# Kernel tuning notes

Hardware: AMD Instinct MI355X
Metric: run time of the kernel (lower is better)

The kernel has to match this reference:

```python
import jax, jax.numpy as jnp
import numpy as np


def _h(s):
    # Step function: 0 where s > 0, else 1 (zero gradient everywhere).
    return jnp.where(s > 0, 0.0, 1.0).astype(s.dtype)


def setup_inputs() -> dict:
    key = jax.random.key(0)
    k1, k2, k3 = jax.random.split(key, 3)
    B, T = 4096, 2048
    x = jax.random.normal(k1, (B, T, 1), dtype=jnp.float32)
    out_prev = jax.random.normal(k2, (B, 1, 1), dtype=jnp.float32)
    lstm_outs = jax.random.normal(k3, (B, T, 4), dtype=jnp.float32)
    return {"x": x, "out_prev": out_prev, "lstm_outs": lstm_outs}


def reference(x, out_prev, lstm_outs):
    # x: [B, T, 1], out_prev: [B, 1, 1] (only first step used), lstm_outs: [B, T, 4]
    xT = jnp.swapaxes(x, 0, 1)          # [T, B, 1]
    wT = jnp.swapaxes(lstm_outs, 0, 1)  # [T, B, 4]

    def step(prev, inputs):
        # prev: [B, 1]
        xt, wt = inputs                  # [B, 1], [B, 4]
        m_lo = wt[:, 0:1]
        m_up = wt[:, 1:2]
        c_lo = wt[:, 2:3]
        c_up = wt[:, 3:4]
        # h() arguments use detached weights in the original (grad is zero through
        # the step function anyway); stop_gradient kept for faithfulness.
        m_lo_d = jax.lax.stop_gradient(m_lo)
        m_up_d = jax.lax.stop_gradient(m_up)
        c_lo_d = jax.lax.stop_gradient(c_lo)
        c_up_d = jax.lax.stop_gradient(c_up)
        f1 = _h((m_lo_d * xt + m_lo_d * c_lo_d - prev) / m_lo_d)
        f2 = _h((prev - m_up_d * xt - m_up_d * c_up_d) / m_up_d)
        out = (m_lo * xt * f1 + m_lo * c_lo * f1
               + m_up * xt * f2 + m_up * c_up * f2
               + prev * (1.0 - f1) * (1.0 - f2))
        return out, out

    init = out_prev[:, 0, :]             # [B, 1]
    _, outs = jax.lax.scan(step, init, (xT, wT))  # outs: [T, B, 1]
    custom_output = jnp.swapaxes(outs, 0, 1)      # [B, T, 1]
    # Original also returns (lstm_outs, 0, 0, 0) passthrough; main output is below.
    return custom_output
```

## Files before the change

### kernel.cpp

```cpp
#include <hip/hip_runtime.h>


#define C 64
#define NCH 32
#define TS 65
#define XS 68

#define WG_BARRIER() asm volatile("s_waitcnt lgkmcnt(0)\ns_barrier" ::: "memory")

__global__ __launch_bounds__(192) void pc_scan(
    const float* __restrict__ x, const float* __restrict__ p0,
    const float4* __restrict__ lstm4, float* __restrict__ out,
    int B, int T) {
#pragma clang fp contract(off)
  __shared__ float4 tileA[2][16 * TS];
  __shared__ float4 tileB[2][16 * TS];
  __shared__ float xt[16 * XS];
  __shared__ float ostg[2][16 * XS];

  const int tid = threadIdx.x;
  const int b0 = blockIdx.x * 16;
  const float4* x4 = reinterpret_cast<const float4*>(x);
  float4* out4 = reinterpret_cast<float4*>(out);

  const int q = tid - 64;
  const int pj = (q >> 3) & 15;
  const int pk = q & 7;

  float4 L00, L01, L02, L03, L04, L05, L06, L07;
  float4 L10, L11, L12, L13, L14, L15, L16, L17;
  float4 X00, X01, X10, X11;

#define ISSUE(S, CH)                                                    \
  if (tid >= 64) {                                                      \
    size_t rb = (size_t)(b0 + pj) * T + (size_t)(CH) * C;               \
    const float4* lp = lstm4 + rb + pk;                                 \
    L##S##0 = lp[0];  L##S##1 = lp[8];  L##S##2 = lp[16];               \
    L##S##3 = lp[24]; L##S##4 = lp[32]; L##S##5 = lp[40];               \
    L##S##6 = lp[48]; L##S##7 = lp[56];                                 \
    X##S##0 = x4[(rb >> 2) + 2 * pk];                                   \
    X##S##1 = x4[(rb >> 2) + 2 * pk + 1];                               \
  }

#define STAGE_ELT(LV, SS, BUF)                                          \
  {                                                                     \
    float4 wv = LV;                       \
    float xv = xt[pj * XS + (SS)];                                      \
    float a1 = wv.x * xv, a2 = wv.x * wv.z;                             \
    float L1v = a1 + a2;                                                \
    unsigned s1m = __float_as_uint(wv.x) & 0x80000000u;                 \
    float L1f = __uint_as_float(__float_as_uint(L1v) ^ s1m);            \
    float a3 = wv.y * xv, a4 = wv.y * wv.w;                             \
    unsigned f2m = (__float_as_uint(wv.y) & 0x80000000u) ^ 0x80000000u; \
    float a3f = __uint_as_float(__float_as_uint(a3) ^ f2m);             \
    float a4f = __uint_as_float(__float_as_uint(a4) ^ f2m);             \
    float V01 = a3 + a4;                                                \
    float V11 = (L1v + a3) + a4;                                        \
    tileA[BUF][pj * TS + (SS)] =                                        \
        make_float4(__uint_as_float(s1m), L1f, __uint_as_float(f2m), a3f); \
    tileB[BUF][pj * TS + (SS)] = make_float4(a4f, V11, V01, L1v);       \
  }

#define STAGE(S, BUF)                                                   \
  if (tid >= 64) {                                                      \
    *(float4*)&xt[pj * XS + 8 * pk] = X##S##0;                          \
    *(float4*)&xt[pj * XS + 8 * pk + 4] = X##S##1;                      \
    STAGE_ELT(L##S##0, pk,      BUF)                                    \
    STAGE_ELT(L##S##1, pk + 8,  BUF)                                    \
    STAGE_ELT(L##S##2, pk + 16, BUF)                                    \
    STAGE_ELT(L##S##3, pk + 24, BUF)                                    \
    STAGE_ELT(L##S##4, pk + 32, BUF)                                    \
    STAGE_ELT(L##S##5, pk + 40, BUF)                                    \
    STAGE_ELT(L##S##6, pk + 48, BUF)                                    \
    STAGE_ELT(L##S##7, pk + 56, BUF)                                    \
  }

#define FLUSH(CP, OB)                                                   \
  if (tid >= 64) {                                                      \
    float4 v0 = *(const float4*)&ostg[OB][pj * XS + 8 * pk];            \
    float4 v1 = *(const float4*)&ostg[OB][pj * XS + 8 * pk + 4];        \
    size_t ob = ((size_t)(b0 + pj) * T + (size_t)(CP) * C) >> 2;        \
    out4[ob + 2 * pk] = v0;                                             \
    out4[ob + 2 * pk + 1] = v1;                                         \
  }

#define SCAN(BUF, OB)                                                   \
  if (tid < 16) {                                                       \
    _Pragma("unroll") for (int s = 0; s < C; ++s) {                     \
      float4 A = tileA[BUF][tid * TS + s];                              \
      float4 Bv = tileB[BUF][tid * TS + s];                             \
      unsigned pu = __float_as_uint(p);                                 \
      float pf = __uint_as_float(pu ^ __float_as_uint(A.x));            \
      bool c1 = pf >= A.y;                                              \
      float pp = __uint_as_float(pu ^ __float_as_uint(A.z));            \
      float qv = pp - A.w;                                              \
      bool c2 = qv >= Bv.x;                                             \
      float i1 = c1 ? Bv.y : Bv.z;                                      \
      float i2 = c1 ? Bv.w : p;                                         \
      p = c2 ? i1 : i2;                                                 \
      ostg[OB][tid * XS + s] = p;                                       \
    }                                                                   \
  }

  float p = (tid < 16) ? p0[b0 + tid] : 0.0f;

  ISSUE(0, 0)
  STAGE(0, 0)
  ISSUE(1, 1)
  WG_BARRIER();

  for (int c = 0; c < NCH; c += 2) {
    if (c + 2 < NCH) ISSUE(0, c + 2)
    STAGE(1, 1)
    if (c >= 1) FLUSH(c - 1, 1)
    SCAN(0, 0)
    WG_BARRIER();

    if (c + 3 < NCH) ISSUE(1, c + 3)
    if (c + 2 < NCH) STAGE(0, 0)
    FLUSH(c, 0)
    SCAN(1, 1)
    WG_BARRIER();
  }
  FLUSH(NCH - 1, 1)
}

extern "C" void kernel_launch(void* const* d_in, const int* in_sizes, int n_in,
                              void* d_out, int out_size, void* d_ws, size_t ws_size,
                              hipStream_t stream) {
  const float* x = (const float*)d_in[0];
  const float* op = (const float*)d_in[1];
  const float4* lstm = (const float4*)d_in[2];
  int B = in_sizes[1];
  int T = in_sizes[0] / B;
  hipLaunchKernelGGL(pc_scan, dim3(B / 16), dim3(192), 0, stream,
                     x, op, lstm, (float*)d_out, B, T);
}
```

Baseline: 237.4 us.

## Halve rows per workgroup and software-pipeline scan LDS reads with vectorized output

Each workgroup now handles 8 batch rows instead of 16, which doubles the grid to B/8 blocks and halves LDS use per block. The producer threads each load 4 float4s per chunk instead of 8, so each producer holds fewer registers. In the serial scan loop, LDS reads are prefetched 8 steps ahead into registers and outputs are written as float4 pairs, taking LDS latency off the dependency chain. The trade-off is that only 8 of the 192 threads do scan work per block, and the extra blocks add scheduling overhead.

```diff
diff --git a/kernel.cpp b/kernel.cpp
--- a/kernel.cpp
+++ b/kernel.cpp
@@ -13,33 +13,31 @@
     const float4* __restrict__ lstm4, float* __restrict__ out,
     int B, int T) {
 #pragma clang fp contract(off)
-  __shared__ float4 tileA[2][16 * TS];
-  __shared__ float4 tileB[2][16 * TS];
-  __shared__ float xt[16 * XS];
-  __shared__ float ostg[2][16 * XS];
+  __shared__ float4 tileA[2][8 * TS];
+  __shared__ float4 tileB[2][8 * TS];
+  __shared__ float xt[8 * XS];
+  __shared__ float ostg[2][8 * XS];
 
   const int tid = threadIdx.x;
-  const int b0 = blockIdx.x * 16;
+  const int b0 = blockIdx.x * 8;
   const float4* x4 = reinterpret_cast<const float4*>(x);
   float4* out4 = reinterpret_cast<float4*>(out);
 
   const int q = tid - 64;
-  const int pj = (q >> 3) & 15;
-  const int pk = q & 7;
+  const int pj = (q >> 4) & 7;
+  const int pk = q & 15;
 
-  float4 L00, L01, L02, L03, L04, L05, L06, L07;
-  float4 L10, L11, L12, L13, L14, L15, L16, L17;
-  float4 X00, X01, X10, X11;
+  float4 L00, L01, L02, L03;
+  float4 L10, L11, L12, L13;
+  float4 X0, X1;
 
 #define ISSUE(S, CH)                                                    \
   if (tid >= 64) {                                                      \
     size_t rb = (size_t)(b0 + pj) * T + (size_t)(CH) * C;               \
     const float4* lp = lstm4 + rb + pk;                                 \
-    L##S##0 = lp[0];  L##S##1 = lp[8];  L##S##2 = lp[16];               \
-    L##S##3 = lp[24]; L##S##4 = lp[32]; L##S##5 = lp[40];               \
-    L##S##6 = lp[48]; L##S##7 = lp[56];                                 \
-    X##S##0 = x4[(rb >> 2) + 2 * pk];                                   \
-    X##S##1 = x4[(rb >> 2) + 2 * pk + 1];                               \
+    L##S##0 = lp[0];  L##S##1 = lp[16];                                 \
+    L##S##2 = lp[32]; L##S##3 = lp[48];                                 \
+    X##S = x4[(rb >> 2) + pk];                                          \
   }
 
 #define STAGE_ELT(LV, SS, BUF)                                          \
@@ -63,46 +61,58 @@
 
 #define STAGE(S, BUF)                                                   \
   if (tid >= 64) {                                                      \
-    *(float4*)&xt[pj * XS + 8 * pk] = X##S##0;                          \
-    *(float4*)&xt[pj * XS + 8 * pk + 4] = X##S##1;                      \
+    *(float4*)&xt[pj * XS + 4 * pk] = X##S;                             \
     STAGE_ELT(L##S##0, pk,      BUF)                                    \
-    STAGE_ELT(L##S##1, pk + 8,  BUF)                                    \
-    STAGE_ELT(L##S##2, pk + 16, BUF)                                    \
-    STAGE_ELT(L##S##3, pk + 24, BUF)                                    \
-    STAGE_ELT(L##S##4, pk + 32, BUF)                                    \
-    STAGE_ELT(L##S##5, pk + 40, BUF)                                    \
-    STAGE_ELT(L##S##6, pk + 48, BUF)                                    \
-    STAGE_ELT(L##S##7, pk + 56, BUF)                                    \
+    STAGE_ELT(L##S##1, pk + 16, BUF)                                    \
+    STAGE_ELT(L##S##2, pk + 32, BUF)                                    \
+    STAGE_ELT(L##S##3, pk + 48, BUF)                                    \
   }
 
 #define FLUSH(CP, OB)                                                   \
   if (tid >= 64) {                                                      \
-    float4 v0 = *(const float4*)&ostg[OB][pj * XS + 8 * pk];            \
-    float4 v1 = *(const float4*)&ostg[OB][pj * XS + 8 * pk + 4];        \
-    size_t ob = ((size_t)(b0 + pj) * T + (size_t)(CP) * C) >> 2;        \
-    out4[ob + 2 * pk] = v0;                                             \
-    out4[ob + 2 * pk + 1] = v1;                                         \
+    float4 v = *(const float4*)&ostg[OB][pj * XS + 4 * pk];             \
+    out4[(((size_t)(b0 + pj) * T + (size_t)(CP) * C) >> 2) + pk] = v;   \
+  }
+
+#define RSTEP(I, OVC)                                                   \
+  {                                                                     \
+    float4 A = rA##I;                                                   \
+    float4 Bv = rB##I;                                                  \
+    if (g < 7) {                                                        \
+      rA##I = ta[8 * g + 8 + I];                                        \
+      rB##I = tb[8 * g + 8 + I];                                        \
+    }                                                                   \
+    unsigned pu = __float_as_uint(p);                                   \
+    float pf = __uint_as_float(pu ^ __float_as_uint(A.x));              \
+    bool c1 = pf >= A.y;                                                \
+    float pp = __uint_as_float(pu ^ __float_as_uint(A.z));              \
+    float qv = pp - A.w;                                                \
+    bool c2 = qv >= Bv.x;                                               \
+    float i1 = c1 ? Bv.y : Bv.z;                                        \
+    float i2 = c1 ? Bv.w : p;                                           \
+    p = c2 ? i1 : i2;                                                   \
+    OVC = p;                                                            \
   }
 
 #define SCAN(BUF, OB)                                                   \
-  if (tid < 16) {                                                       \
-    _Pragma("unroll") for (int s = 0; s < C; ++s) {                     \
-      float4 A = tileA[BUF][tid * TS + s];                              \
-      float4 Bv = tileB[BUF][tid * TS + s];                             \
-      unsigned pu = __float_as_uint(p);                                 \
-      float pf = __uint_as_float(pu ^ __float_as_uint(A.x));            \
-      bool c1 = pf >= A.y;                                              \
-      float pp = __uint_as_float(pu ^ __float_as_uint(A.z));            \
-      float qv = pp - A.w;                                              \
-      bool c2 = qv >= Bv.x;                                             \
-      float i1 = c1 ? Bv.y : Bv.z;                                      \
-      float i2 = c1 ? Bv.w : p;                                         \
-      p = c2 ? i1 : i2;                                                 \
-      ostg[OB][tid * XS + s] = p;                                       \
+  if (tid < 8) {                                                        \
+    const float4* ta = &tileA[BUF][tid * TS];                           \
+    const float4* tb = &tileB[BUF][tid * TS];                           \
+    float* orow = &ostg[OB][tid * XS];                                  \
+    float4 rA0 = ta[0], rA1 = ta[1], rA2 = ta[2], rA3 = ta[3];          \
+    float4 rA4 = ta[4], rA5 = ta[5], rA6 = ta[6], rA7 = ta[7];          \
+    float4 rB0 = tb[0], rB1 = tb[1], rB2 = tb[2], rB3 = tb[3];          \
+    float4 rB4 = tb[4], rB5 = tb[5], rB6 = tb[6], rB7 = tb[7];          \
+    _Pragma("unroll") for (int g = 0; g < 8; ++g) {                     \
+      float4 ov0, ov1;                                                  \
+      RSTEP(0, ov0.x) RSTEP(1, ov0.y) RSTEP(2, ov0.z) RSTEP(3, ov0.w)   \
+      RSTEP(4, ov1.x) RSTEP(5, ov1.y) RSTEP(6, ov1.z) RSTEP(7, ov1.w)   \
+      *(float4*)&orow[8 * g] = ov0;                                     \
+      *(float4*)&orow[8 * g + 4] = ov1;                                 \
     }                                                                   \
   }
 
-  float p = (tid < 16) ? p0[b0 + tid] : 0.0f;
+  float p = (tid < 8) ? p0[b0 + tid] : 0.0f;
 
   ISSUE(0, 0)
   STAGE(0, 0)
@@ -133,6 +143,6 @@
   const float4* lstm = (const float4*)d_in[2];
   int B = in_sizes[1];
   int T = in_sizes[0] / B;
-  hipLaunchKernelGGL(pc_scan, dim3(B / 16), dim3(192), 0, stream,
+  hipLaunchKernelGGL(pc_scan, dim3(B / 8), dim3(192), 0, stream,
                      x, op, lstm, (float*)d_out, B, T);
 }
```

Result: no change. 237.2 us (-0.1%).

## Replace workgroup barriers with LDS flag producer-consumer handoff between waves

Applied to the files above, without the earlier changes.

Replaces the per-chunk workgroup barriers with LDS flag signalling. The two producer waves mark each staged chunk, and the scan wave publishes a progress counter. Tile buffers grow to three and output staging to four, so producers can run further ahead while the scanner works. The scan loop also software-prefetches the next tile entries into registers and writes outputs as float4. Spin-waiting with s_sleep adds polling overhead and relies on LDS visibility and ordering within a workgroup, which is only fenced at compiler level.

```diff
diff --git a/kernel.cpp b/kernel.cpp
--- a/kernel.cpp
+++ b/kernel.cpp
@@ -3,36 +3,47 @@
 
 #define C 64
 #define NCH 32
+#define NTB 3
+#define NOB 4
 #define TS 65
 #define XS 68
 
-#define WG_BARRIER() asm volatile("s_waitcnt lgkmcnt(0)\ns_barrier" ::: "memory")
+#define CFENCE() asm volatile("" ::: "memory")
 
 __global__ __launch_bounds__(192) void pc_scan(
     const float* __restrict__ x, const float* __restrict__ p0,
     const float4* __restrict__ lstm4, float* __restrict__ out,
     int B, int T) {
 #pragma clang fp contract(off)
-  __shared__ float4 tileA[2][16 * TS];
-  __shared__ float4 tileB[2][16 * TS];
+  __shared__ float4 tileA[NTB][16 * TS];
+  __shared__ float4 tileB[NTB][16 * TS];
   __shared__ float xt[16 * XS];
-  __shared__ float ostg[2][16 * XS];
+  __shared__ float ostg[NOB][16 * XS];
+  __shared__ int stagedw[2][NCH];
+  __shared__ int scanned;
 
   const int tid = threadIdx.x;
   const int b0 = blockIdx.x * 16;
   const float4* x4 = reinterpret_cast<const float4*>(x);
   float4* out4 = reinterpret_cast<float4*>(out);
 
-  const int q = tid - 64;
-  const int pj = (q >> 3) & 15;
-  const int pk = q & 7;
+  for (int i = tid; i < 2 * NCH; i += 192) ((int*)stagedw)[i] = 0;
+  if (tid == 0) scanned = 0;
+  __syncthreads();
 
-  float4 L00, L01, L02, L03, L04, L05, L06, L07;
-  float4 L10, L11, L12, L13, L14, L15, L16, L17;
-  float4 X00, X01, X10, X11;
+  if (tid >= 64) {
+    const int q = tid - 64;
+    const int pj = (q >> 3) & 15;
+    const int pk = q & 7;
+    const int w = (tid >> 6) - 1;
+    const bool lead = (q & 63) == 0;
+
+    float4 L00, L01, L02, L03, L04, L05, L06, L07;
+    float4 L10, L11, L12, L13, L14, L15, L16, L17;
+    float4 X00, X01, X10, X11;
 
 #define ISSUE(S, CH)                                                    \
-  if (tid >= 64) {                                                      \
+  {                                                                     \
     size_t rb = (size_t)(b0 + pj) * T + (size_t)(CH) * C;               \
     const float4* lp = lstm4 + rb + pk;                                 \
     L##S##0 = lp[0];  L##S##1 = lp[8];  L##S##2 = lp[16];               \
@@ -62,7 +73,7 @@
   }
 
 #define STAGE(S, BUF)                                                   \
-  if (tid >= 64) {                                                      \
+  {                                                                     \
     *(float4*)&xt[pj * XS + 8 * pk] = X##S##0;                          \
     *(float4*)&xt[pj * XS + 8 * pk + 4] = X##S##1;                      \
     STAGE_ELT(L##S##0, pk,      BUF)                                    \
@@ -76,7 +87,7 @@
   }
 
 #define FLUSH(CP, OB)                                                   \
-  if (tid >= 64) {                                                      \
+  {                                                                     \
     float4 v0 = *(const float4*)&ostg[OB][pj * XS + 8 * pk];            \
     float4 v1 = *(const float4*)&ostg[OB][pj * XS + 8 * pk + 4];        \
     size_t ob = ((size_t)(b0 + pj) * T + (size_t)(CP) * C) >> 2;        \
@@ -84,45 +95,83 @@
     out4[ob + 2 * pk + 1] = v1;                                         \
   }
 
-#define SCAN(BUF, OB)                                                   \
-  if (tid < 16) {                                                       \
-    _Pragma("unroll") for (int s = 0; s < C; ++s) {                     \
-      float4 A = tileA[BUF][tid * TS + s];                              \
-      float4 Bv = tileB[BUF][tid * TS + s];                             \
-      unsigned pu = __float_as_uint(p);                                 \
-      float pf = __uint_as_float(pu ^ __float_as_uint(A.x));            \
-      bool c1 = pf >= A.y;                                              \
-      float pp = __uint_as_float(pu ^ __float_as_uint(A.z));            \
-      float qv = pp - A.w;                                              \
-      bool c2 = qv >= Bv.x;                                             \
-      float i1 = c1 ? Bv.y : Bv.z;                                      \
-      float i2 = c1 ? Bv.w : p;                                         \
-      p = c2 ? i1 : i2;                                                 \
-      ostg[OB][tid * XS + s] = p;                                       \
+#define PWAIT(TGT)                                                      \
+  while (*(volatile int*)&scanned < (TGT)) __builtin_amdgcn_s_sleep(1); \
+  CFENCE();
+
+    ISSUE(0, 0)
+    ISSUE(1, 1)
+
+    for (int k = 0; k < NCH; k += 2) {
+      PWAIT(k - 2)
+      STAGE(0, k % NTB)
+      CFENCE();
+      if (lead) *(volatile int*)&stagedw[w][k] = 1;
+      if (k + 2 < NCH) ISSUE(0, k + 2)
+      if (k >= 3) FLUSH(k - 3, (k - 3) % NOB)
+      PWAIT(k - 1)
+      STAGE(1, (k + 1) % NTB)
+      CFENCE();
+      if (lead) *(volatile int*)&stagedw[w][k + 1] = 1;
+      if (k + 3 < NCH) ISSUE(1, k + 3)
+      if (k >= 2) FLUSH(k - 2, (k - 2) % NOB)
+    }
+    for (int j = NCH - 3; j < NCH; ++j) {
+      PWAIT(j + 1)
+      FLUSH(j, j % NOB)
+    }
+  } else {
+    float p = (tid < 16) ? p0[b0 + tid] : 0.0f;
+
+#define RSTEP(I, OVC)                                                   \
+  {                                                                     \
+    float4 A = rA##I;                                                   \
+    float4 Bv = rB##I;                                                  \
+    if (g < 7) {                                                        \
+      rA##I = ta[8 * g + 8 + I];                                        \
+      rB##I = tb[8 * g + 8 + I];                                        \
     }                                                                   \
+    unsigned pu = __float_as_uint(p);                                   \
+    float pf = __uint_as_float(pu ^ __float_as_uint(A.x));              \
+    bool c1 = pf >= A.y;                                                \
+    float pp = __uint_as_float(pu ^ __float_as_uint(A.z));              \
+    float qv = pp - A.w;                                                \
+    bool c2 = qv >= Bv.x;                                               \
+    float i1 = c1 ? Bv.y : Bv.z;                                        \
+    float i2 = c1 ? Bv.w : p;                                           \
+    p = c2 ? i1 : i2;                                                   \
+    OVC = p;                                                            \
   }
 
-  float p = (tid < 16) ? p0[b0 + tid] : 0.0f;
-
-  ISSUE(0, 0)
-  STAGE(0, 0)
-  ISSUE(1, 1)
-  WG_BARRIER();
-
-  for (int c = 0; c < NCH; c += 2) {
-    if (c + 2 < NCH) ISSUE(0, c + 2)
-    STAGE(1, 1)
-    if (c >= 1) FLUSH(c - 1, 1)
-    SCAN(0, 0)
-    WG_BARRIER();
-
-    if (c + 3 < NCH) ISSUE(1, c + 3)
-    if (c + 2 < NCH) STAGE(0, 0)
-    FLUSH(c, 0)
-    SCAN(1, 1)
-    WG_BARRIER();
+    for (int c = 0; c < NCH; ++c) {
+      for (;;) {
+        int a = *(volatile int*)&stagedw[0][c];
+        int b = *(volatile int*)&stagedw[1][c];
+        if (a + b == 2) break;
+        __builtin_amdgcn_s_sleep(1);
+      }
+      CFENCE();
+      if (tid < 16) {
+        const float4* ta = &tileA[c % NTB][tid * TS];
+        const float4* tb = &tileB[c % NTB][tid * TS];
+        float* orow = &ostg[c % NOB][tid * XS];
+        float4 rA0 = ta[0], rA1 = ta[1], rA2 = ta[2], rA3 = ta[3];
+        float4 rA4 = ta[4], rA5 = ta[5], rA6 = ta[6], rA7 = ta[7];
+        float4 rB0 = tb[0], rB1 = tb[1], rB2 = tb[2], rB3 = tb[3];
+        float4 rB4 = tb[4], rB5 = tb[5], rB6 = tb[6], rB7 = tb[7];
+#pragma unroll
+        for (int g = 0; g < 8; ++g) {
+          float4 ov0, ov1;
+          RSTEP(0, ov0.x) RSTEP(1, ov0.y) RSTEP(2, ov0.z) RSTEP(3, ov0.w)
+          RSTEP(4, ov1.x) RSTEP(5, ov1.y) RSTEP(6, ov1.z) RSTEP(7, ov1.w)
+          *(float4*)&orow[8 * g] = ov0;
+          *(float4*)&orow[8 * g + 4] = ov1;
+        }
+      }
+      CFENCE();
+      if (tid == 0) *(volatile int*)&scanned = c + 1;
+    }
   }
-  FLUSH(NCH - 1, 1)
 }
 
 extern "C" void kernel_launch(void* const* d_in, const int* in_sizes, int n_in,
```

After: 230.6 us. 2.9% less time.
